# Kernel optimization log

Hardware: AMD Instinct MI355X
Metric: run time of the kernel (lower is better)

The kernel has to match this reference:

```python
import jax, jax.numpy as jnp
import numpy as np

INPUT_SIZE = 4096
HIDDEN = 1024
WINDOW = 2048
STRIDE = 1024
METRIC = 32
POOLING = "last"


def setup_inputs() -> dict:
    key = jax.random.key(0)
    ks = jax.random.split(key, 9)
    s = 1.0 / np.sqrt(HIDDEN)  # torch LSTMCell/Linear init bound
    u = lambda k, shape: jax.random.uniform(k, shape, jnp.float32, -s, s)
    return {
        "inp": jax.random.normal(ks[0], (WINDOW, INPUT_SIZE), jnp.float32),
        "h1": jax.random.normal(ks[1], (1, HIDDEN), jnp.float32),
        "c1": jax.random.normal(ks[2], (1, HIDDEN), jnp.float32),
        "W_ih": u(ks[3], (4 * HIDDEN, INPUT_SIZE)),
        "W_hh": u(ks[4], (4 * HIDDEN, HIDDEN)),
        "b_ih": u(ks[5], (4 * HIDDEN,)),
        "b_hh": u(ks[6], (4 * HIDDEN,)),
        "fc_w": u(ks[7], (METRIC, HIDDEN)),
        "fc_b": u(ks[8], (METRIC,)),
    }


def reference(inp, h1, c1, W_ih, W_hh, b_ih, b_hh, fc_w, fc_b):
    window = min(WINDOW, inp.shape[0])
    # Precompute the input-side gate projection as one GEMM: [T, 4H]
    xg = inp[:window] @ W_ih.T + b_ih

    def step(carry, xg_t):
        h, c = carry  # each [1, H]
        gates = xg_t + h @ W_hh.T + b_hh  # [1, 4H]
        i, f, g, o = jnp.split(gates, 4, axis=-1)
        c = jax.nn.sigmoid(f) * c + jax.nn.sigmoid(i) * jnp.tanh(g)
        h = jax.nn.sigmoid(o) * jnp.tanh(c)
        return (h, c), (h, c)

    (h_fin, c_fin), (hs, cs) = jax.lax.scan(step, (h1, c1), xg)

    if window >= STRIDE:
        h_last = jax.lax.stop_gradient(hs[STRIDE - 1])  # [1, H], detached
        c_last = jax.lax.stop_gradient(cs[STRIDE - 1])
    else:
        h_last, c_last = None, None

    if POOLING == "mean":
        # mean of fc(h_i) over last STRIDE steps of the window
        out = (hs[window - STRIDE:, 0, :] @ fc_w.T + fc_b).sum(axis=0, keepdims=True) / STRIDE
    else:  # 'last'
        out = h_fin @ fc_w.T + fc_b  # [1, METRIC]
    out = jnp.tanh(out)
    return out, h_last, c_last
```

## Files before the change

kernel.cpp:

```cpp
#include <hip/hip_runtime.h>
#include <stdint.h>

typedef unsigned short u16;
typedef unsigned long long u64;
typedef __attribute__((ext_vector_type(8))) short short8;
typedef __attribute__((ext_vector_type(4))) float floatx4;
typedef __attribute__((ext_vector_type(4))) unsigned int u32x4;

#define K_IN    4096
#define HID     1024
#define G4H     4096
#define T_STEPS 2048
#define NWG     128
#define SPIN_MAX 60000

__device__ __forceinline__ u16 f2bf(float f) {
  union { float f; unsigned int i; } v; v.f = f;
  unsigned int lsb = (v.i >> 16) & 1u;
  v.i += 0x7fffu + lsb;
  return (u16)(v.i >> 16);
}
__device__ __forceinline__ float finz(float x) {
  unsigned b = __float_as_uint(x);
  return ((b & 0x7f800000u) == 0x7f800000u) ? 0.f : x;
}
__device__ __forceinline__ float sigm(float x) {
  x = fminf(30.f, fmaxf(-30.f, finz(x)));
  return 1.0f / (1.0f + __expf(-x));
}
__device__ __forceinline__ float tanh_s(float x) {
  x = fminf(15.f, fmaxf(-15.f, finz(x)));
  float e = __expf(2.0f * x);
  return (e - 1.0f) / (e + 1.0f);
}

__device__ __forceinline__ void publish_h(u64* hx, int slot, int idx, float h) {
  h = finz(h);
  u64 v = ((u64)(unsigned)(slot + 1) << 32) | (u64)__float_as_uint(h);
  __hip_atomic_store(&hx[(size_t)slot * HID + idx], v,
                     __ATOMIC_RELAXED, __HIP_MEMORY_SCOPE_AGENT);
}

__device__ __forceinline__ void poll2(const u64* hx, int slot, int j0,
                                      float* v, int* alive) {
  const u64* p = hx + (size_t)slot * HID + j0;
  const unsigned tag = (unsigned)(slot + 1);
  if (*alive) {
    int spins = 0;
    for (;;) {
      u32x4 r;
      asm volatile("global_load_dwordx4 %0, %1, off sc0 sc1\n\t"
                   "s_waitcnt vmcnt(0)"
                   : "=&v"(r) : "v"(p) : "memory");
      if (r.y == tag && r.w == tag) {
        v[0] = finz(__uint_as_float(r.x));
        v[1] = finz(__uint_as_float(r.z));
        return;
      }
      if (++spins > SPIN_MAX) { *alive = 0; break; }
      __builtin_amdgcn_s_sleep(1);
    }
  }
  v[0] = v[1] = 0.f;
}

__global__ __launch_bounds__(256) void cvt_bf16_k(const float* __restrict__ src,
                                                  u16* __restrict__ dst, int n4) {
  int i = blockIdx.x * 256 + threadIdx.x;
  if (i < n4) {
    float4 v = *(const float4*)(src + (size_t)i * 4);
    u16 o0 = f2bf(v.x), o1 = f2bf(v.y), o2 = f2bf(v.z), o3 = f2bf(v.w);
    ushort4 o = {o0, o1, o2, o3};
    *(ushort4*)(dst + (size_t)i * 4) = o;
  }
}

#define GLD_LDS16(gsrc, ldst)                                             \
  __builtin_amdgcn_global_load_lds(                                       \
      (const __attribute__((address_space(1))) void*)(gsrc),              \
      (__attribute__((address_space(3))) void*)(ldst), 16, 0, 0)

__global__ __launch_bounds__(256) void xg_gemm_k(const u16* __restrict__ A,
                                                 const u16* __restrict__ B,
                                                 const float* __restrict__ bias,
                                                 float* __restrict__ C)
{
  __shared__ __align__(16) u16 As[128 * 64];
  __shared__ __align__(16) u16 Bs[128 * 64];
  const int tid  = threadIdx.x;
  const int lane = tid & 63;
  const int quad = lane >> 4;
  const int l16  = lane & 15;
  const int wid  = tid >> 6;
  const int wm   = wid >> 1, wn = wid & 1;
  const int tileM = blockIdx.y * 128;
  const int tileN = blockIdx.x * 128;

  floatx4 acc[4][4];
  #pragma unroll
  for (int mi = 0; mi < 4; ++mi)
    #pragma unroll
    for (int ni = 0; ni < 4; ++ni)
      acc[mi][ni] = (floatx4){0.f, 0.f, 0.f, 0.f};

  for (int k0 = 0; k0 < K_IN; k0 += 64) {
    #pragma unroll
    for (int i = 0; i < 4; ++i) {
      int c   = i * 256 + tid;
      int row = c >> 3, col = (c & 7) * 8;
      int cb  = i * 256 + wid * 64;
      GLD_LDS16(A + (size_t)(tileM + row) * K_IN + k0 + col, As + (size_t)cb * 8);
      GLD_LDS16(B + (size_t)(tileN + row) * K_IN + k0 + col, Bs + (size_t)cb * 8);
    }
    __syncthreads();
    #pragma unroll
    for (int kk = 0; kk < 64; kk += 32) {
      short8 av[4], bv[4];
      #pragma unroll
      for (int mi = 0; mi < 4; ++mi)
        av[mi] = *(const short8*)(As + (wm * 64 + mi * 16 + l16) * 64 + kk + quad * 8);
      #pragma unroll
      for (int ni = 0; ni < 4; ++ni)
        bv[ni] = *(const short8*)(Bs + (wn * 64 + ni * 16 + l16) * 64 + kk + quad * 8);
      #pragma unroll
      for (int mi = 0; mi < 4; ++mi)
        #pragma unroll
        for (int ni = 0; ni < 4; ++ni)
          acc[mi][ni] = __builtin_amdgcn_mfma_f32_16x16x32_bf16(av[mi], bv[ni], acc[mi][ni], 0, 0, 0);
    }
    __syncthreads();
  }
  #pragma unroll
  for (int ni = 0; ni < 4; ++ni) {
    int n = tileN + wn * 64 + ni * 16 + l16;
    float bn = bias[n];
    #pragma unroll
    for (int mi = 0; mi < 4; ++mi) {
      int mbase = tileM + wm * 64 + mi * 16 + quad * 4;
      #pragma unroll
      for (int r = 0; r < 4; ++r)
        C[(size_t)(mbase + r) * G4H + n] = acc[mi][ni][r] + bn;
    }
  }
}

__global__ __launch_bounds__(512, 1) void lstm_scan_k(const float* __restrict__ Whh,
                                                      const float* __restrict__ bhh,
                                                      const float* __restrict__ h1,
                                                      const float* __restrict__ c1,
                                                      const float* __restrict__ fcw,
                                                      const float* __restrict__ fcb,
                                                      const float* __restrict__ xg,
                                                      u64* hx,
                                                      float* out)
{
  const int g    = blockIdx.x;
  const int tid  = threadIdx.x;
  const int lane = tid & 63;
  const int w    = tid >> 6;
  const int u    = g * 8 + w;

  __shared__ __align__(16) float h_local[HID];
  __shared__ float hpub[8];
  __shared__ float xgb[2][32];
  __shared__ float pp[32][16];

  floatx4 wreg[4][4];
  #pragma unroll
  for (int q = 0; q < 4; ++q) {
    const float* wr = Whh + (size_t)(q * HID + u) * HID;
    #pragma unroll
    for (int j = 0; j < 4; ++j)
      wreg[q][j] = *(const floatx4*)(wr + j * 256 + lane * 4);
  }
  const float bh0 = bhh[u], bh1 = bhh[HID + u], bh2 = bhh[2 * HID + u], bh3 = bhh[3 * HID + u];

  float c_state = c1[u];
  if (tid < 8) publish_h(hx, 0, g * 8 + tid, h1[g * 8 + tid]);

  int alive = 1;
  const int j0 = tid * 2;
  for (int t = 0; t < T_STEPS; ++t) {
    float xval = 0.f;
    if (tid < 32) xval = finz(xg[(size_t)t * G4H + (tid >> 3) * HID + g * 8 + (tid & 7)]);
    float v[2];
    poll2(hx, t, j0, v, &alive);
    h_local[j0 + 0] = v[0]; h_local[j0 + 1] = v[1];
    if (tid < 32) xgb[t & 1][tid] = xval;
    __syncthreads();

    float s0 = 0.f, s1 = 0.f, s2 = 0.f, s3 = 0.f;
    #pragma unroll
    for (int j = 0; j < 4; ++j) {
      floatx4 hv = *(const floatx4*)(h_local + j * 256 + lane * 4);
      #pragma unroll
      for (int k = 0; k < 4; ++k) {
        s0 = fmaf(wreg[0][j][k], hv[k], s0);
        s1 = fmaf(wreg[1][j][k], hv[k], s1);
        s2 = fmaf(wreg[2][j][k], hv[k], s2);
        s3 = fmaf(wreg[3][j][k], hv[k], s3);
      }
    }

#define DPP_LEVEL(mods) \
    asm("v_add_f32 %0, %0, %0 " mods : "+v"(s0)); \
    asm("v_add_f32 %0, %0, %0 " mods : "+v"(s1)); \
    asm("v_add_f32 %0, %0, %0 " mods : "+v"(s2)); \
    asm("v_add_f32 %0, %0, %0 " mods : "+v"(s3));
    DPP_LEVEL("row_shr:1 bound_ctrl:0")
    DPP_LEVEL("row_shr:2 bound_ctrl:0")
    DPP_LEVEL("row_shr:4 bank_mask:0xe")
    DPP_LEVEL("row_shr:8 bank_mask:0xc")
    DPP_LEVEL("row_bcast:15 row_mask:0xa")
    DPP_LEVEL("row_bcast:31 row_mask:0xc")
#undef DPP_LEVEL

    if (lane == 63) {
      const float* xb = xgb[t & 1];
      float gi = s0 + xb[w]      + bh0;
      float gf = s1 + xb[8 + w]  + bh1;
      float gg = s2 + xb[16 + w] + bh2;
      float go = s3 + xb[24 + w] + bh3;
      float iv = sigm(gi), fv = sigm(gf), gv = tanh_s(gg), ov = sigm(go);
      c_state = finz(fv * c_state + iv * gv);
      float hval = ov * tanh_s(c_state);
      hpub[w] = hval;
      if (t == 1023) {
        out[32 + u]       = finz(hval);
        out[32 + HID + u] = finz(c_state);
      }
    }
    __syncthreads();

    if (tid < 8) publish_h(hx, t + 1, g * 8 + tid, hpub[tid]);
  }

  if (g == 0) {
    float v[2];
    poll2(hx, T_STEPS, j0, v, &alive);
    h_local[j0 + 0] = v[0]; h_local[j0 + 1] = v[1];
    __syncthreads();
    const int m = tid >> 4, seg = tid & 15;
    float pacc = 0.f;
    for (int k = seg * 64; k < seg * 64 + 64; ++k)
      pacc = fmaf(fcw[m * HID + k], h_local[k], pacc);
    pp[m][seg] = finz(pacc);
    __syncthreads();
    if (tid < 32) {
      float sum = fcb[tid];
      #pragma unroll
      for (int i = 0; i < 16; ++i) sum += pp[tid][i];
      out[tid] = tanh_s(finz(sum));
    }
  }
}

extern "C" void kernel_launch(void* const* d_in, const int* in_sizes, int n_in,
                              void* d_out, int out_size, void* d_ws, size_t ws_size,
                              hipStream_t stream) {
  const float* inp = (const float*)d_in[0];
  const float* h1  = (const float*)d_in[1];
  const float* c1  = (const float*)d_in[2];
  const float* Wih = (const float*)d_in[3];
  const float* Whh = (const float*)d_in[4];
  const float* bih = (const float*)d_in[5];
  const float* bhh = (const float*)d_in[6];
  const float* fcw = (const float*)d_in[7];
  const float* fcb = (const float*)d_in[8];
  float* out = (float*)d_out;

  const size_t xg_bytes  = (size_t)T_STEPS * G4H * 4;
  const size_t hx_bytes  = (size_t)(T_STEPS + 1) * HID * 8;
  const size_t ab_bytes  = (size_t)T_STEPS * K_IN * 2;
  const size_t wb_bytes  = (size_t)G4H * K_IN * 2;
  if (ws_size < xg_bytes + hx_bytes + ab_bytes + wb_bytes) return;

  float* xg   = (float*)d_ws;
  u64*   hx   = (u64*)((char*)d_ws + xg_bytes);
  u16*   Abf  = (u16*)((char*)d_ws + xg_bytes + hx_bytes);
  u16*   Wbf  = (u16*)((char*)d_ws + xg_bytes + hx_bytes + ab_bytes);

  const int nA4 = T_STEPS * K_IN / 4;
  const int nW4 = G4H * K_IN / 4;
  cvt_bf16_k<<<dim3((nA4 + 255) / 256), 256, 0, stream>>>(inp, Abf, nA4);
  cvt_bf16_k<<<dim3((nW4 + 255) / 256), 256, 0, stream>>>(Wih, Wbf, nW4);
  xg_gemm_k<<<dim3(G4H / 128, T_STEPS / 128), 256, 0, stream>>>(Abf, Wbf, bih, xg);
  lstm_scan_k<<<dim3(NWG), 512, 0, stream>>>(Whh, bhh, h1, c1, fcw, fcb, xg, hx, out);
}
```

Before: 4.748 ms.

## Fuse input GEMM and LSTM scan into one kernel with tagged xg handoff

Merges the bf16 conversion, the input-projection GEMM and the recurrent scan into a single launch. 128 blocks run the GEMM row-tile by row-tile and publish each xg value tagged with its timestep, while another 128 blocks run the scan and spin on those tags, so the scan can start before the whole GEMM is done. The separate bf16 conversion kernels go away because conversion now happens inline during tile loads. The cost is that only 4 of 8 waves do MFMA work, the GEMM no longer uses async global-to-LDS loads, xg storage doubles to 64-bit tagged entries, and the tile order (row-major over M in passes of 128) has to keep pace with the scan's consumption.

```diff
diff --git a/kernel.cpp b/kernel.cpp
--- a/kernel.cpp
+++ b/kernel.cpp
@@ -34,12 +34,12 @@
   return (e - 1.0f) / (e + 1.0f);
 }
 
-__device__ __forceinline__ void publish_h(u64* hx, int slot, int idx, float h) {
-  h = finz(h);
-  u64 v = ((u64)(unsigned)(slot + 1) << 32) | (u64)__float_as_uint(h);
-  __hip_atomic_store(&hx[(size_t)slot * HID + idx], v,
-                     __ATOMIC_RELAXED, __HIP_MEMORY_SCOPE_AGENT);
-}
+__device__ __forceinline__ void publish_u64(u64* p, unsigned tag, float v) {
+  v = finz(v);
+  u64 e = ((u64)tag << 32) | (u64)__float_as_uint(v);
+  __hip_atomic_store(p, e, __ATOMIC_RELAXED, __HIP_MEMORY_SCOPE_AGENT);
+}
+#define HXLD(addr) __hip_atomic_load((addr), __ATOMIC_RELAXED, __HIP_MEMORY_SCOPE_AGENT)
 
 __device__ __forceinline__ void poll2(const u64* hx, int slot, int j0,
                                       float* v, int* alive) {
@@ -64,106 +64,116 @@
   v[0] = v[1] = 0.f;
 }
 
-__global__ __launch_bounds__(256) void cvt_bf16_k(const float* __restrict__ src,
-                                                  u16* __restrict__ dst, int n4) {
-  int i = blockIdx.x * 256 + threadIdx.x;
-  if (i < n4) {
-    float4 v = *(const float4*)(src + (size_t)i * 4);
-    u16 o0 = f2bf(v.x), o1 = f2bf(v.y), o2 = f2bf(v.z), o3 = f2bf(v.w);
-    ushort4 o = {o0, o1, o2, o3};
-    *(ushort4*)(dst + (size_t)i * 4) = o;
-  }
-}
-
-#define GLD_LDS16(gsrc, ldst)                                             \
-  __builtin_amdgcn_global_load_lds(                                       \
-      (const __attribute__((address_space(1))) void*)(gsrc),              \
-      (__attribute__((address_space(3))) void*)(ldst), 16, 0, 0)
-
-__global__ __launch_bounds__(256) void xg_gemm_k(const u16* __restrict__ A,
-                                                 const u16* __restrict__ B,
-                                                 const float* __restrict__ bias,
-                                                 float* __restrict__ C)
+__device__ __forceinline__ short8 cvt8(float4 a, float4 b) {
+  short8 r;
+  r[0] = (short)f2bf(a.x); r[1] = (short)f2bf(a.y);
+  r[2] = (short)f2bf(a.z); r[3] = (short)f2bf(a.w);
+  r[4] = (short)f2bf(b.x); r[5] = (short)f2bf(b.y);
+  r[6] = (short)f2bf(b.z); r[7] = (short)f2bf(b.w);
+  return r;
+}
+
+__global__ __launch_bounds__(512, 1) void fused_k(const float* __restrict__ inp,
+                                                  const float* __restrict__ Wih,
+                                                  const float* __restrict__ bih,
+                                                  const float* __restrict__ Whh,
+                                                  const float* __restrict__ bhh,
+                                                  const float* __restrict__ h1,
+                                                  const float* __restrict__ c1,
+                                                  const float* __restrict__ fcw,
+                                                  const float* __restrict__ fcb,
+                                                  u64* xgx,
+                                                  u64* hx,
+                                                  float* out)
 {
-  __shared__ __align__(16) u16 As[128 * 64];
-  __shared__ __align__(16) u16 Bs[128 * 64];
-  const int tid  = threadIdx.x;
-  const int lane = tid & 63;
-  const int quad = lane >> 4;
-  const int l16  = lane & 15;
-  const int wid  = tid >> 6;
-  const int wm   = wid >> 1, wn = wid & 1;
-  const int tileM = blockIdx.y * 128;
-  const int tileN = blockIdx.x * 128;
-
-  floatx4 acc[4][4];
-  #pragma unroll
-  for (int mi = 0; mi < 4; ++mi)
-    #pragma unroll
-    for (int ni = 0; ni < 4; ++ni)
-      acc[mi][ni] = (floatx4){0.f, 0.f, 0.f, 0.f};
-
-  for (int k0 = 0; k0 < K_IN; k0 += 64) {
-    #pragma unroll
-    for (int i = 0; i < 4; ++i) {
-      int c   = i * 256 + tid;
-      int row = c >> 3, col = (c & 7) * 8;
-      int cb  = i * 256 + wid * 64;
-      GLD_LDS16(A + (size_t)(tileM + row) * K_IN + k0 + col, As + (size_t)cb * 8);
-      GLD_LDS16(B + (size_t)(tileN + row) * K_IN + k0 + col, Bs + (size_t)cb * 8);
-    }
-    __syncthreads();
-    #pragma unroll
-    for (int kk = 0; kk < 64; kk += 32) {
-      short8 av[4], bv[4];
-      #pragma unroll
-      for (int mi = 0; mi < 4; ++mi)
-        av[mi] = *(const short8*)(As + (wm * 64 + mi * 16 + l16) * 64 + kk + quad * 8);
-      #pragma unroll
-      for (int ni = 0; ni < 4; ++ni)
-        bv[ni] = *(const short8*)(Bs + (wn * 64 + ni * 16 + l16) * 64 + kk + quad * 8);
+  __shared__ __align__(16) char smem[33 * 1024];
+  const int bid = blockIdx.x;
+  const int tid = threadIdx.x;
+
+  if (bid < NWG) {
+    u16* As = (u16*)smem;
+    u16* Bs = (u16*)(smem + 16384);
+    const int lane = tid & 63;
+    const int quad = lane >> 4;
+    const int l16  = lane & 15;
+    const int wid  = tid >> 6;
+    const int wm   = (wid >> 1) & 1, wn = wid & 1;
+
+    for (int pass = 0; pass < 4; ++pass) {
+      const int id = bid + pass * NWG;
+      const int tileM = (id >> 5) * 128;
+      const int tileN = (id & 31) * 128;
+
+      floatx4 acc[4][4];
       #pragma unroll
       for (int mi = 0; mi < 4; ++mi)
         #pragma unroll
         for (int ni = 0; ni < 4; ++ni)
-          acc[mi][ni] = __builtin_amdgcn_mfma_f32_16x16x32_bf16(av[mi], bv[ni], acc[mi][ni], 0, 0, 0);
-    }
-    __syncthreads();
-  }
-  #pragma unroll
-  for (int ni = 0; ni < 4; ++ni) {
-    int n = tileN + wn * 64 + ni * 16 + l16;
-    float bn = bias[n];
-    #pragma unroll
-    for (int mi = 0; mi < 4; ++mi) {
-      int mbase = tileM + wm * 64 + mi * 16 + quad * 4;
-      #pragma unroll
-      for (int r = 0; r < 4; ++r)
-        C[(size_t)(mbase + r) * G4H + n] = acc[mi][ni][r] + bn;
-    }
-  }
-}
-
-__global__ __launch_bounds__(512, 1) void lstm_scan_k(const float* __restrict__ Whh,
-                                                      const float* __restrict__ bhh,
-                                                      const float* __restrict__ h1,
-                                                      const float* __restrict__ c1,
-                                                      const float* __restrict__ fcw,
-                                                      const float* __restrict__ fcb,
-                                                      const float* __restrict__ xg,
-                                                      u64* hx,
-                                                      float* out)
-{
-  const int g    = blockIdx.x;
-  const int tid  = threadIdx.x;
+          acc[mi][ni] = (floatx4){0.f, 0.f, 0.f, 0.f};
+
+      for (int k0 = 0; k0 < K_IN; k0 += 64) {
+        #pragma unroll
+        for (int i = 0; i < 2; ++i) {
+          int c = i * 512 + tid;
+          int row = c >> 3, colg = (c & 7) * 8;
+          const float* pa = inp + (size_t)(tileM + row) * K_IN + k0 + colg;
+          const float* pb = Wih + (size_t)(tileN + row) * K_IN + k0 + colg;
+          float4 a0 = *(const float4*)pa, a1 = *(const float4*)(pa + 4);
+          float4 b0 = *(const float4*)pb, b1 = *(const float4*)(pb + 4);
+          *(short8*)(As + c * 8) = cvt8(a0, a1);
+          *(short8*)(Bs + c * 8) = cvt8(b0, b1);
+        }
+        __syncthreads();
+        if (wid < 4) {
+          #pragma unroll
+          for (int kk = 0; kk < 64; kk += 32) {
+            short8 av[4], bv[4];
+            #pragma unroll
+            for (int mi = 0; mi < 4; ++mi)
+              av[mi] = *(const short8*)(As + (wm * 64 + mi * 16 + l16) * 64 + kk + quad * 8);
+            #pragma unroll
+            for (int ni = 0; ni < 4; ++ni)
+              bv[ni] = *(const short8*)(Bs + (wn * 64 + ni * 16 + l16) * 64 + kk + quad * 8);
+            #pragma unroll
+            for (int mi = 0; mi < 4; ++mi)
+              #pragma unroll
+              for (int ni = 0; ni < 4; ++ni)
+                acc[mi][ni] = __builtin_amdgcn_mfma_f32_16x16x32_bf16(av[mi], bv[ni], acc[mi][ni], 0, 0, 0);
+          }
+        }
+        __syncthreads();
+      }
+      if (wid < 4) {
+        #pragma unroll
+        for (int ni = 0; ni < 4; ++ni) {
+          int n = tileN + wn * 64 + ni * 16 + l16;
+          float bn = bih[n];
+          #pragma unroll
+          for (int mi = 0; mi < 4; ++mi) {
+            int mbase = tileM + wm * 64 + mi * 16 + quad * 4;
+            #pragma unroll
+            for (int r = 0; r < 4; ++r) {
+              int row = mbase + r;
+              publish_u64(&xgx[(size_t)row * G4H + n], (unsigned)(row + 1),
+                          acc[mi][ni][r] + bn);
+            }
+          }
+        }
+      }
+      __syncthreads();
+    }
+    return;
+  }
+
+  const int g    = bid - NWG;
   const int lane = tid & 63;
   const int w    = tid >> 6;
   const int u    = g * 8 + w;
 
-  __shared__ __align__(16) float h_local[HID];
-  __shared__ float hpub[8];
-  __shared__ float xgb[2][32];
-  __shared__ float pp[32][16];
+  float* h_local = (float*)smem;
+  float* hpub    = (float*)(smem + 4096);
+  float* xgb     = (float*)(smem + 4128);
+  float* pp      = (float*)(smem + 4384);
 
   floatx4 wreg[4][4];
   #pragma unroll
@@ -176,17 +186,34 @@
   const float bh0 = bhh[u], bh1 = bhh[HID + u], bh2 = bhh[2 * HID + u], bh3 = bhh[3 * HID + u];
 
   float c_state = c1[u];
-  if (tid < 8) publish_h(hx, 0, g * 8 + tid, h1[g * 8 + tid]);
+  if (tid < 8) publish_u64(&hx[(size_t)0 * HID + g * 8 + tid], 1u, h1[g * 8 + tid]);
 
   int alive = 1;
   const int j0 = tid * 2;
+  const size_t xoff = (size_t)(tid >> 3) * HID + g * 8 + (tid & 7);
   for (int t = 0; t < T_STEPS; ++t) {
-    float xval = 0.f;
-    if (tid < 32) xval = finz(xg[(size_t)t * G4H + (tid >> 3) * HID + g * 8 + (tid & 7)]);
+    u64 xraw = 0;
+    if (tid < 32) xraw = HXLD(&xgx[(size_t)t * G4H + xoff]);
     float v[2];
     poll2(hx, t, j0, v, &alive);
     h_local[j0 + 0] = v[0]; h_local[j0 + 1] = v[1];
-    if (tid < 32) xgb[t & 1][tid] = xval;
+    if (tid < 32) {
+      const unsigned xtag = (unsigned)(t + 1);
+      float xval;
+      if ((unsigned)(xraw >> 32) == xtag) {
+        xval = finz(__uint_as_float((unsigned)xraw));
+      } else {
+        const u64* p = &xgx[(size_t)t * G4H + xoff];
+        int spins = 0; xval = 0.f;
+        while (alive) {
+          u64 a = HXLD(p);
+          if ((unsigned)(a >> 32) == xtag) { xval = finz(__uint_as_float((unsigned)a)); break; }
+          if (++spins > SPIN_MAX) { alive = 0; break; }
+          __builtin_amdgcn_s_sleep(1);
+        }
+      }
+      xgb[(t & 1) * 32 + tid] = xval;
+    }
     __syncthreads();
 
     float s0 = 0.f, s1 = 0.f, s2 = 0.f, s3 = 0.f;
@@ -216,7 +243,7 @@
 #undef DPP_LEVEL
 
     if (lane == 63) {
-      const float* xb = xgb[t & 1];
+      const float* xb = xgb + (t & 1) * 32;
       float gi = s0 + xb[w]      + bh0;
       float gf = s1 + xb[8 + w]  + bh1;
       float gg = s2 + xb[16 + w] + bh2;
@@ -232,7 +259,8 @@
     }
     __syncthreads();
 
-    if (tid < 8) publish_h(hx, t + 1, g * 8 + tid, hpub[tid]);
+    if (tid < 8) publish_u64(&hx[(size_t)(t + 1) * HID + g * 8 + tid],
+                             (unsigned)(t + 2), hpub[tid]);
   }
 
   if (g == 0) {
@@ -244,12 +272,12 @@
     float pacc = 0.f;
     for (int k = seg * 64; k < seg * 64 + 64; ++k)
       pacc = fmaf(fcw[m * HID + k], h_local[k], pacc);
-    pp[m][seg] = finz(pacc);
+    pp[m * 16 + seg] = finz(pacc);
     __syncthreads();
     if (tid < 32) {
       float sum = fcb[tid];
       #pragma unroll
-      for (int i = 0; i < 16; ++i) sum += pp[tid][i];
+      for (int i = 0; i < 16; ++i) sum += pp[tid * 16 + i];
       out[tid] = tanh_s(finz(sum));
     }
   }
@@ -269,21 +297,13 @@
   const float* fcb = (const float*)d_in[8];
   float* out = (float*)d_out;
 
-  const size_t xg_bytes  = (size_t)T_STEPS * G4H * 4;
+  const size_t xgx_bytes = (size_t)T_STEPS * G4H * 8;
   const size_t hx_bytes  = (size_t)(T_STEPS + 1) * HID * 8;
-  const size_t ab_bytes  = (size_t)T_STEPS * K_IN * 2;
-  const size_t wb_bytes  = (size_t)G4H * K_IN * 2;
-  if (ws_size < xg_bytes + hx_bytes + ab_bytes + wb_bytes) return;
-
-  float* xg   = (float*)d_ws;
-  u64*   hx   = (u64*)((char*)d_ws + xg_bytes);
-  u16*   Abf  = (u16*)((char*)d_ws + xg_bytes + hx_bytes);
-  u16*   Wbf  = (u16*)((char*)d_ws + xg_bytes + hx_bytes + ab_bytes);
-
-  const int nA4 = T_STEPS * K_IN / 4;
-  const int nW4 = G4H * K_IN / 4;
-  cvt_bf16_k<<<dim3((nA4 + 255) / 256), 256, 0, stream>>>(inp, Abf, nA4);
-  cvt_bf16_k<<<dim3((nW4 + 255) / 256), 256, 0, stream>>>(Wih, Wbf, nW4);
-  xg_gemm_k<<<dim3(G4H / 128, T_STEPS / 128), 256, 0, stream>>>(Abf, Wbf, bih, xg);
-  lstm_scan_k<<<dim3(NWG), 512, 0, stream>>>(Whh, bhh, h1, c1, fcw, fcb, xg, hx, out);
-}
+  if (ws_size < xgx_bytes + hx_bytes) return;
+
+  u64* xgx = (u64*)d_ws;
+  u64* hx  = (u64*)((char*)d_ws + xgx_bytes);
+
+  fused_k<<<dim3(2 * NWG), 512, 0, stream>>>(inp, Wih, bih, Whh, bhh, h1, c1,
+                                             fcw, fcb, xgx, hx, out);
+}
```

New measurement: 4.798 ms. About the same (+1.1%).
